# Kernel optimization log

Hardware: AMD Instinct MI355X
Metric: run time of the kernel (lower is better)

## Reference

```python
import jax, jax.numpy as jnp
import numpy as np

N = 100000       # num_nodes
E = 800000       # num edges (avg degree 8)
EMB = 64         # emb_dim
HID = 256        # hidden_dim


def setup_inputs() -> dict:
    key = jax.random.key(0)
    k1, k2, k3, k4, k5, k6, k7 = jax.random.split(key, 7)
    def xavier(k, fan_in, fan_out):
        limit = float(np.sqrt(6.0 / (fan_in + fan_out)))
        return jax.random.uniform(k, (fan_in, fan_out), jnp.float32, -limit, limit)
    return {
        "row": jax.random.randint(k1, (E,), 0, N, dtype=jnp.int64) if jax.config.jax_enable_x64 else jax.random.randint(k1, (E,), 0, N).astype(jnp.int32),
        "col": jax.random.randint(k2, (E,), 0, N).astype(jnp.int32),
        "val": jax.random.uniform(k3, (E,), jnp.float32),
        "emb": jax.random.normal(k4, (N, EMB), jnp.float32) * 0.02,
        "W0": xavier(k5, EMB, HID),
        "W1": xavier(k6, HID, HID),
        "W2": xavier(k7, HID, HID),
    }


def reference(row, col, val, emb, W0, W1, W2):
    # SpMM: out[r] = sum_{edges e with row[e]==r} val[e] * emb[col[e]]
    msgs = val[:, None] * emb[col]                      # [E, EMB] gather + scale
    x = jax.ops.segment_sum(msgs, row, num_segments=N)  # [N, EMB] scatter-add
    # MLP (bias-free linears; dropout=0.0 / eval mode => identity)
    x = jax.nn.relu(x @ W0)   # [N, HID]
    x = jax.nn.relu(x @ W1)   # [N, HID]
    x = x @ W2                # [N, HID]
    return x
```

## Files before the change

kernel.cpp:

```cpp
#include <hip/hip_runtime.h>
#include <hip/hip_bf16.h>

#define EMB 64
#define HID 256

typedef __attribute__((ext_vector_type(8))) short short8_t;
typedef __attribute__((ext_vector_type(4))) float f32x4;

__device__ __forceinline__ unsigned short f2bf(float f)
{
    union { float f; unsigned int u; } c; c.f = f;
    unsigned int u = c.u;
    u += 0x7fffu + ((u >> 16) & 1u);
    return (unsigned short)(u >> 16);
}
__device__ __forceinline__ float bf2f(unsigned short b)
{
    union { unsigned int u; float f; } c; c.u = ((unsigned int)b) << 16;
    return c.f;
}

__global__ __launch_bounds__(256) void prep_kernel(
    const float* __restrict__ emb, const float* __restrict__ W0,
    const float* __restrict__ W1, const float* __restrict__ W2,
    int* __restrict__ counts, unsigned short* __restrict__ embb,
    unsigned short* __restrict__ W0f, unsigned short* __restrict__ W1f,
    unsigned short* __restrict__ W2f, int M, int zb, int cb)
{
    int b = blockIdx.x;
    if (b < zb) {
        int idx = (b * 256 + threadIdx.x) * 4;
        if (idx + 3 < M) {
            int4 z; z.x = 0; z.y = 0; z.z = 0; z.w = 0;
            *(int4*)&counts[idx] = z;
        } else {
            for (int i = idx; i < M; ++i) counts[i] = 0;
        }
        return;
    }
    b -= zb;
    if (b < cb) {
        int idx = (b * 256 + threadIdx.x) * 4;
        if (idx + 3 < M * EMB) {
            float4 v = *(const float4*)&emb[idx];
            ushort4 o;
            o.x = f2bf(v.x); o.y = f2bf(v.y); o.z = f2bf(v.z); o.w = f2bf(v.w);
            *(ushort4*)&embb[idx] = o;
        }
        return;
    }
    b -= cb;
    if (b < 8) {
        int i    = b * 256 + threadIdx.x;
        int lane = i & 63;
        int kc   = (i >> 6) & 1;
        int nt   = i >> 7;
        int lr   = lane & 15, kg = lane >> 4;
        unsigned short tmp[8];
#pragma unroll
        for (int j = 0; j < 8; ++j)
            tmp[j] = f2bf(W0[(kc * 32 + kg * 8 + j) * HID + nt * 16 + lr]);
        *(short8_t*)&W0f[(size_t)i * 8] = *(short8_t*)tmp;
        return;
    }
    b -= 8;
    if (b < 32) {
        int i    = b * 256 + threadIdx.x;
        int lane = i & 63;
        int kc   = (i >> 6) & 7;
        int nt   = i >> 9;
        int lr   = lane & 15, kg = lane >> 4;
        unsigned short tmp[8];
#pragma unroll
        for (int j = 0; j < 8; ++j)
            tmp[j] = f2bf(W1[(kc * 32 + kg * 8 + j) * HID + nt * 16 + lr]);
        *(short8_t*)&W1f[(size_t)i * 8] = *(short8_t*)tmp;
        return;
    }
    b -= 32;
    {
        int i    = b * 256 + threadIdx.x;
        int lane = i & 63;
        int kc   = (i >> 6) & 7;
        int nt   = i >> 9;
        int lr   = lane & 15, kg = lane >> 4;
        unsigned short tmp[8];
#pragma unroll
        for (int j = 0; j < 8; ++j)
            tmp[j] = f2bf(W2[(kc * 32 + kg * 8 + j) * HID + nt * 16 + lr]);
        *(short8_t*)&W2f[(size_t)i * 8] = *(short8_t*)tmp;
    }
}

__global__ __launch_bounds__(256) void hist_kernel(
    const int* __restrict__ row, int* __restrict__ counts, int E)
{
    int base = (blockIdx.x * 256 + threadIdx.x) * 4;
    if (base + 3 < E) {
        int4 r4 = *(const int4*)&row[base];
        atomicAdd(&counts[r4.x], 1);
        atomicAdd(&counts[r4.y], 1);
        atomicAdd(&counts[r4.z], 1);
        atomicAdd(&counts[r4.w], 1);
    } else {
        for (int i = base; i < E; ++i) atomicAdd(&counts[row[i]], 1);
    }
}

__global__ __launch_bounds__(256) void scan_phase1(
    const int* __restrict__ counts, int* __restrict__ excl,
    int* __restrict__ blockSums, int n)
{
    __shared__ int s[256];
    int t = threadIdx.x;
    int base = blockIdx.x * 1024 + t * 4;
    int4 v = {0, 0, 0, 0};
    if (base + 3 < n) {
        v = *(const int4*)&counts[base];
    } else {
        if (base + 0 < n) v.x = counts[base + 0];
        if (base + 1 < n) v.y = counts[base + 1];
        if (base + 2 < n) v.z = counts[base + 2];
        if (base + 3 < n) v.w = counts[base + 3];
    }
    int tsum = v.x + v.y + v.z + v.w;
    s[t] = tsum;
    __syncthreads();
#pragma unroll
    for (int off = 1; off < 256; off <<= 1) {
        int val = (t >= off) ? s[t - off] : 0;
        __syncthreads();
        s[t] += val;
        __syncthreads();
    }
    if (t == 255) blockSums[blockIdx.x] = s[255];
    int e0 = s[t] - tsum;
    int e1 = e0 + v.x;
    int e2 = e1 + v.y;
    int e3 = e2 + v.z;
    if (base + 0 < n) excl[base + 0] = e0;
    if (base + 1 < n) excl[base + 1] = e1;
    if (base + 2 < n) excl[base + 2] = e2;
    if (base + 3 < n) excl[base + 3] = e3;
}

__global__ __launch_bounds__(256) void scan_phase2(int* blockSums, int nb)
{
    __shared__ int s[256];
    int t = threadIdx.x;
    int v = (t < nb) ? blockSums[t] : 0;
    s[t] = v;
    __syncthreads();
#pragma unroll
    for (int off = 1; off < 256; off <<= 1) {
        int val = (t >= off) ? s[t - off] : 0;
        __syncthreads();
        s[t] += val;
        __syncthreads();
    }
    if (t < nb) blockSums[t] = s[t] - v;
}

__global__ __launch_bounds__(256) void scan_phase3(
    int* __restrict__ offsets, const int* __restrict__ blockSums,
    int* __restrict__ cursor, int n)
{
    int i = blockIdx.x * 256 + threadIdx.x;
    if (i >= n) return;
    int o = offsets[i] + blockSums[i >> 10];
    offsets[i] = o;
    cursor[i]  = o;
}

__global__ __launch_bounds__(256) void scatter_kernel(
    const int* __restrict__ row, const int* __restrict__ col,
    const float* __restrict__ val, int* __restrict__ cursor,
    uint2* __restrict__ edata, int E)
{
    int e = blockIdx.x * 256 + threadIdx.x;
    if (e >= E) return;
    int r = row[e];
    int pos = atomicAdd(&cursor[r], 1);
    uint2 d;
    d.x = (unsigned)col[e];
    d.y = __float_as_uint(val[e]);
    edata[pos] = d;
}

__global__ __launch_bounds__(256) void pull_kernel(
    const int* __restrict__ offsets, const int* __restrict__ counts,
    const uint2* __restrict__ edata, const unsigned short* __restrict__ embb,
    unsigned short* __restrict__ xb, int Nn)
{
    int r    = blockIdx.x * 4 + (threadIdx.x >> 6);
    int lane = threadIdx.x & 63;
    if (r >= Nn) return;
    int beg = offsets[r];
    int cnt = counts[r];
    float acc = 0.f;
    for (int i = 0; i < cnt; i += 8) {
        uint2 ed[8];
#pragma unroll
        for (int j = 0; j < 8; ++j) {
            int idx = i + j;
            idx = (idx < cnt) ? idx : (cnt - 1);
            ed[j] = edata[beg + idx];
        }
        float g[8];
#pragma unroll
        for (int j = 0; j < 8; ++j)
            g[j] = bf2f(embb[(size_t)ed[j].x * EMB + lane]);
#pragma unroll
        for (int j = 0; j < 8; ++j) {
            float v = (i + j < cnt) ? __uint_as_float(ed[j].y) : 0.f;
            acc += v * g[j];
        }
    }
    xb[(size_t)r * EMB + lane] = f2bf(acc);
}

__global__ __launch_bounds__(256) void mlp_fused(
    const unsigned short* __restrict__ xb,
    const unsigned short* __restrict__ W0f,
    const unsigned short* __restrict__ W1f,
    const unsigned short* __restrict__ W2f,
    float* __restrict__ out, int M)
{
    __shared__ unsigned short H[64 * 256];

    const int t    = threadIdx.x;
    const int lane = t & 63;
    const int w    = t >> 6;
    const int lr   = lane & 15;
    const int kg   = lane >> 4;
    const int row0 = blockIdx.x * 64;
    char* Hb = (char*)H;

#define HOFF(row, bytecol) ((((row) * 512) + (bytecol)) ^ (((row) & 7) << 4))

    short8_t ax[2][4];
#pragma unroll
    for (int kc = 0; kc < 2; ++kc)
#pragma unroll
        for (int m = 0; m < 4; ++m) {
            int gr = row0 + m * 16 + lr;
            ax[kc][m] = *(const short8_t*)(xb + (size_t)(gr < M ? gr : 0) * EMB
                                           + kc * 32 + kg * 8);
        }
    f32x4 acc[4][4] = {};
#pragma unroll
    for (int kc = 0; kc < 2; ++kc) {
        short8_t b[4];
#pragma unroll
        for (int n = 0; n < 4; ++n)
            b[n] = *(const short8_t*)&W0f[(size_t)(((w * 4 + n) * 2 + kc) * 64 + lane) * 8];
#pragma unroll
        for (int m = 0; m < 4; ++m)
#pragma unroll
            for (int n = 0; n < 4; ++n)
                acc[m][n] = __builtin_amdgcn_mfma_f32_16x16x32_bf16(
                    ax[kc][m], b[n], acc[m][n], 0, 0, 0);
    }
#pragma unroll
    for (int m = 0; m < 4; ++m)
#pragma unroll
        for (int r = 0; r < 4; ++r)
#pragma unroll
            for (int n = 0; n < 4; ++n)
                *(unsigned short*)(Hb + HOFF(m * 16 + kg * 4 + r,
                                             (w * 64 + n * 16 + lr) * 2)) =
                    f2bf(fmaxf(acc[m][n][r], 0.f));
    __syncthreads();

    f32x4 acc2[4][4] = {};
#pragma unroll
    for (int kc = 0; kc < 8; ++kc) {
        short8_t a[4], b[4];
#pragma unroll
        for (int n = 0; n < 4; ++n)
            b[n] = *(const short8_t*)&W1f[(size_t)(((w * 4 + n) * 8 + kc) * 64 + lane) * 8];
#pragma unroll
        for (int m = 0; m < 4; ++m)
            a[m] = *(const short8_t*)(Hb + HOFF(m * 16 + lr, kc * 64 + kg * 16));
#pragma unroll
        for (int m = 0; m < 4; ++m)
#pragma unroll
            for (int n = 0; n < 4; ++n)
                acc2[m][n] = __builtin_amdgcn_mfma_f32_16x16x32_bf16(
                    a[m], b[n], acc2[m][n], 0, 0, 0);
    }
    __syncthreads();
#pragma unroll
    for (int m = 0; m < 4; ++m)
#pragma unroll
        for (int r = 0; r < 4; ++r)
#pragma unroll
            for (int n = 0; n < 4; ++n)
                *(unsigned short*)(Hb + HOFF(m * 16 + kg * 4 + r,
                                             (w * 64 + n * 16 + lr) * 2)) =
                    f2bf(fmaxf(acc2[m][n][r], 0.f));
    __syncthreads();

    f32x4 acc3[4][4] = {};
#pragma unroll
    for (int kc = 0; kc < 8; ++kc) {
        short8_t a[4], b[4];
#pragma unroll
        for (int n = 0; n < 4; ++n)
            b[n] = *(const short8_t*)&W2f[(size_t)(((w * 4 + n) * 8 + kc) * 64 + lane) * 8];
#pragma unroll
        for (int m = 0; m < 4; ++m)
            a[m] = *(const short8_t*)(Hb + HOFF(m * 16 + lr, kc * 64 + kg * 16));
#pragma unroll
        for (int m = 0; m < 4; ++m)
#pragma unroll
            for (int n = 0; n < 4; ++n)
                acc3[m][n] = __builtin_amdgcn_mfma_f32_16x16x32_bf16(
                    a[m], b[n], acc3[m][n], 0, 0, 0);
    }
#pragma unroll
    for (int m = 0; m < 4; ++m)
#pragma unroll
        for (int r = 0; r < 4; ++r) {
            int gr = row0 + m * 16 + kg * 4 + r;
            if (gr < M)
#pragma unroll
                for (int n = 0; n < 4; ++n)
                    out[(size_t)gr * HID + w * 64 + n * 16 + lr] = acc3[m][n][r];
        }
#undef HOFF
}

__global__ __launch_bounds__(256) void spmm_kernel(
    const int* __restrict__ row, const int* __restrict__ col,
    const float* __restrict__ val, const float* __restrict__ emb,
    float* __restrict__ x, int E)
{
    int gid  = blockIdx.x * blockDim.x + threadIdx.x;
    int e    = gid >> 6;
    int lane = gid & 63;
    if (e >= E) return;
    unsafeAtomicAdd(&x[(size_t)row[e] * EMB + lane],
                    val[e] * emb[(size_t)col[e] * EMB + lane]);
}

template<int K, bool RELU>
__global__ __launch_bounds__(256) void gemm_f32(
    const float* A, const float* __restrict__ B, float* C, int M)
{
    __shared__ float As[64][17];
    __shared__ float Bs[16][256];

    const int t    = threadIdx.x;
    const int tn   = t & 15;
    const int row0 = blockIdx.x * 64;
    const int sk = t & 15;
    const int sm = (t >> 4) * 4;

    float acc[4][16];
#pragma unroll
    for (int i = 0; i < 4; ++i)
#pragma unroll
        for (int j = 0; j < 16; ++j) acc[i][j] = 0.f;

    const int mB = ((t & 63) >> 4) * 4;
    const int wq = t >> 6;
    const int myM = (wq * 16) + mB;

    for (int k0 = 0; k0 < K; k0 += 16) {
        __syncthreads();
#pragma unroll
        for (int i = 0; i < 4; ++i) {
            int m  = sm + i;
            int gr = row0 + m;
            As[m][sk] = (gr < M) ? A[(size_t)gr * K + k0 + sk] : 0.f;
        }
#pragma unroll
        for (int r = 0; r < 16; ++r)
            Bs[r][t] = B[(size_t)(k0 + r) * 256 + t];
        __syncthreads();

#pragma unroll
        for (int kk = 0; kk < 16; ++kk) {
            float a0 = As[myM + 0][kk];
            float a1 = As[myM + 1][kk];
            float a2 = As[myM + 2][kk];
            float a3 = As[myM + 3][kk];
            float4 b[4];
#pragma unroll
            for (int j = 0; j < 4; ++j)
                b[j] = *(const float4*)&Bs[kk][tn * 4 + j * 64];
#pragma unroll
            for (int j = 0; j < 4; ++j) {
                acc[0][j*4+0] += a0 * b[j].x;  acc[0][j*4+1] += a0 * b[j].y;
                acc[0][j*4+2] += a0 * b[j].z;  acc[0][j*4+3] += a0 * b[j].w;
                acc[1][j*4+0] += a1 * b[j].x;  acc[1][j*4+1] += a1 * b[j].y;
                acc[1][j*4+2] += a1 * b[j].z;  acc[1][j*4+3] += a1 * b[j].w;
                acc[2][j*4+0] += a2 * b[j].x;  acc[2][j*4+1] += a2 * b[j].y;
                acc[2][j*4+2] += a2 * b[j].z;  acc[2][j*4+3] += a2 * b[j].w;
                acc[3][j*4+0] += a3 * b[j].x;  acc[3][j*4+1] += a3 * b[j].y;
                acc[3][j*4+2] += a3 * b[j].z;  acc[3][j*4+3] += a3 * b[j].w;
            }
        }
    }

#pragma unroll
    for (int i = 0; i < 4; ++i) {
        int gr = row0 + myM + i;
        if (gr < M) {
#pragma unroll
            for (int j = 0; j < 4; ++j) {
                float4 o;
                o.x = acc[i][j*4+0]; o.y = acc[i][j*4+1];
                o.z = acc[i][j*4+2]; o.w = acc[i][j*4+3];
                if (RELU) {
                    o.x = fmaxf(o.x, 0.f); o.y = fmaxf(o.y, 0.f);
                    o.z = fmaxf(o.z, 0.f); o.w = fmaxf(o.w, 0.f);
                }
                *(float4*)&C[(size_t)gr * 256 + tn * 4 + j * 64] = o;
            }
        }
    }
}

extern "C" void kernel_launch(void* const* d_in, const int* in_sizes, int n_in,
                              void* d_out, int out_size, void* d_ws, size_t ws_size,
                              hipStream_t stream)
{
    const int*   row = (const int*)d_in[0];
    const int*   col = (const int*)d_in[1];
    const float* val = (const float*)d_in[2];
    const float* emb = (const float*)d_in[3];
    const float* W0  = (const float*)d_in[4];
    const float* W1  = (const float*)d_in[5];
    const float* W2  = (const float*)d_in[6];
    float* out = (float*)d_out;

    const int E = in_sizes[0];
    const int M = in_sizes[3] / EMB;

    char* ws = (char*)d_ws;

    size_t off = 0;
    auto alloc = [&](size_t bytes) { size_t o = off; off = (off + bytes + 255) & ~(size_t)255; return o; };
    const size_t off_counts = alloc((size_t)M * 4);
    const size_t off_offs   = alloc((size_t)M * 4);
    const size_t off_cursor = alloc((size_t)M * 4);
    const size_t off_bsums  = alloc(1024);
    const size_t off_edata  = alloc((size_t)E * 8);
    const size_t off_embb   = alloc((size_t)M * EMB * 2);
    const size_t off_xb     = alloc((size_t)M * EMB * 2);
    const size_t off_w0     = alloc((size_t)EMB * HID * 2);
    const size_t off_w1     = alloc((size_t)HID * HID * 2);
    const size_t off_w2     = alloc((size_t)HID * HID * 2);
    const size_t need       = off;

    int gblocks = (M + 63) / 64;

    if (ws_size >= need) {
        int*   counts = (int*)(ws + off_counts);
        int*   offs   = (int*)(ws + off_offs);
        int*   cursor = (int*)(ws + off_cursor);
        int*   bsums  = (int*)(ws + off_bsums);
        uint2* edata  = (uint2*)(ws + off_edata);
        unsigned short* embb = (unsigned short*)(ws + off_embb);
        unsigned short* xb  = (unsigned short*)(ws + off_xb);
        unsigned short* W0f = (unsigned short*)(ws + off_w0);
        unsigned short* W1f = (unsigned short*)(ws + off_w1);
        unsigned short* W2f = (unsigned short*)(ws + off_w2);

        int zb = (M / 4 + 255) / 256;
        int cb = ((M * EMB) / 4 + 255) / 256;
        int prep_blocks = zb + cb + 8 + 32 + 32;
        prep_kernel<<<prep_blocks, 256, 0, stream>>>(
            emb, W0, W1, W2, counts, embb, W0f, W1f, W2f, M, zb, cb);

        hist_kernel<<<(E / 4 + 255) / 256, 256, 0, stream>>>(row, counts, E);
        int nb = (M + 1023) / 1024;
        scan_phase1<<<nb, 256, 0, stream>>>(counts, offs, bsums, M);
        scan_phase2<<<1, 256, 0, stream>>>(bsums, nb);
        scan_phase3<<<(M + 255) / 256, 256, 0, stream>>>(offs, bsums, cursor, M);
        scatter_kernel<<<(E + 255) / 256, 256, 0, stream>>>(row, col, val, cursor, edata, E);

        pull_kernel<<<(M + 3) / 4, 256, 0, stream>>>(offs, counts, edata, embb, xb, M);

        mlp_fused<<<gblocks, 256, 0, stream>>>(xb, W0f, W1f, W2f, out, M);
    } else {
        float* x = (float*)ws;
        (void)hipMemsetAsync(x, 0, (size_t)M * EMB * sizeof(float), stream);
        spmm_kernel<<<(E + 3) / 4, 256, 0, stream>>>(row, col, val, emb, x, E);
        gemm_f32<EMB, true ><<<gblocks, 256, 0, stream>>>(x,   W0, out, M);
        gemm_f32<HID, true ><<<gblocks, 256, 0, stream>>>(out, W1, out, M);
        gemm_f32<HID, false><<<gblocks, 256, 0, stream>>>(out, W2, out, M);
    }
}
```

Measured before the change: 201.0 us.

## Grid-stride pull kernel, halve MLP row tile, stage output through LDS

The pull kernel becomes a grid-stride loop where each wave handles about 8 rows and prefetches the next row's offset and count. The fused MLP now works on 32-row tiles instead of 64, which halves LDS and register use per block and doubles the block count. The final fp32 output is staged through shared memory so each lane writes 16-byte vectors instead of scattered 4-byte stores. Costs are an extra barrier and LDS round trip in the epilogue, and weight fragments are reloaded across twice as many blocks.

```diff
diff --git a/kernel.cpp b/kernel.cpp
--- a/kernel.cpp
+++ b/kernel.cpp
@@ -187,36 +187,46 @@
     edata[pos] = d;
 }
 
+#define ROWS_PER_WAVE 8
 __global__ __launch_bounds__(256) void pull_kernel(
     const int* __restrict__ offsets, const int* __restrict__ counts,
     const uint2* __restrict__ edata, const unsigned short* __restrict__ embb,
     unsigned short* __restrict__ xb, int Nn)
 {
-    int r    = blockIdx.x * 4 + (threadIdx.x >> 6);
-    int lane = threadIdx.x & 63;
-    if (r >= Nn) return;
-    int beg = offsets[r];
-    int cnt = counts[r];
-    float acc = 0.f;
-    for (int i = 0; i < cnt; i += 8) {
-        uint2 ed[8];
-#pragma unroll
-        for (int j = 0; j < 8; ++j) {
-            int idx = i + j;
-            idx = (idx < cnt) ? idx : (cnt - 1);
-            ed[j] = edata[beg + idx];
-        }
-        float g[8];
-#pragma unroll
-        for (int j = 0; j < 8; ++j)
-            g[j] = bf2f(embb[(size_t)ed[j].x * EMB + lane]);
-#pragma unroll
-        for (int j = 0; j < 8; ++j) {
-            float v = (i + j < cnt) ? __uint_as_float(ed[j].y) : 0.f;
-            acc += v * g[j];
-        }
-    }
-    xb[(size_t)r * EMB + lane] = f2bf(acc);
+    const int nw   = gridDim.x * 4;
+    const int wid  = blockIdx.x * 4 + (threadIdx.x >> 6);
+    const int lane = threadIdx.x & 63;
+    if (wid >= Nn) return;
+
+    int beg = offsets[wid];
+    int cnt = counts[wid];
+    for (int r = wid; r < Nn; r += nw) {
+        int rn = r + nw;
+        int begN = 0, cntN = 0;
+        if (rn < Nn) { begN = offsets[rn]; cntN = counts[rn]; }
+
+        float acc = 0.f;
+        for (int i = 0; i < cnt; i += 8) {
+            uint2 ed[8];
+#pragma unroll
+            for (int j = 0; j < 8; ++j) {
+                int idx = i + j;
+                idx = (idx < cnt) ? idx : (cnt - 1);
+                ed[j] = edata[beg + idx];
+            }
+            float g[8];
+#pragma unroll
+            for (int j = 0; j < 8; ++j)
+                g[j] = bf2f(embb[(size_t)ed[j].x * EMB + lane]);
+#pragma unroll
+            for (int j = 0; j < 8; ++j) {
+                float v = (i + j < cnt) ? __uint_as_float(ed[j].y) : 0.f;
+                acc += v * g[j];
+            }
+        }
+        xb[(size_t)r * EMB + lane] = f2bf(acc);
+        beg = begN; cnt = cntN;
+    }
 }
 
 __global__ __launch_bounds__(256) void mlp_fused(
@@ -226,28 +236,28 @@
     const unsigned short* __restrict__ W2f,
     float* __restrict__ out, int M)
 {
-    __shared__ unsigned short H[64 * 256];
+    __shared__ unsigned short H[32 * 256];
 
     const int t    = threadIdx.x;
     const int lane = t & 63;
     const int w    = t >> 6;
     const int lr   = lane & 15;
     const int kg   = lane >> 4;
-    const int row0 = blockIdx.x * 64;
+    const int row0 = blockIdx.x * 32;
     char* Hb = (char*)H;
 
 #define HOFF(row, bytecol) ((((row) * 512) + (bytecol)) ^ (((row) & 7) << 4))
 
-    short8_t ax[2][4];
+    short8_t ax[2][2];
 #pragma unroll
     for (int kc = 0; kc < 2; ++kc)
 #pragma unroll
-        for (int m = 0; m < 4; ++m) {
+        for (int m = 0; m < 2; ++m) {
             int gr = row0 + m * 16 + lr;
             ax[kc][m] = *(const short8_t*)(xb + (size_t)(gr < M ? gr : 0) * EMB
                                            + kc * 32 + kg * 8);
         }
-    f32x4 acc[4][4] = {};
+    f32x4 acc[2][4] = {};
 #pragma unroll
     for (int kc = 0; kc < 2; ++kc) {
         short8_t b[4];
@@ -255,14 +265,14 @@
         for (int n = 0; n < 4; ++n)
             b[n] = *(const short8_t*)&W0f[(size_t)(((w * 4 + n) * 2 + kc) * 64 + lane) * 8];
 #pragma unroll
-        for (int m = 0; m < 4; ++m)
+        for (int m = 0; m < 2; ++m)
 #pragma unroll
             for (int n = 0; n < 4; ++n)
                 acc[m][n] = __builtin_amdgcn_mfma_f32_16x16x32_bf16(
                     ax[kc][m], b[n], acc[m][n], 0, 0, 0);
     }
 #pragma unroll
-    for (int m = 0; m < 4; ++m)
+    for (int m = 0; m < 2; ++m)
 #pragma unroll
         for (int r = 0; r < 4; ++r)
 #pragma unroll
@@ -272,18 +282,18 @@
                     f2bf(fmaxf(acc[m][n][r], 0.f));
     __syncthreads();
 
-    f32x4 acc2[4][4] = {};
+    f32x4 acc2[2][4] = {};
 #pragma unroll
     for (int kc = 0; kc < 8; ++kc) {
-        short8_t a[4], b[4];
+        short8_t a[2], b[4];
 #pragma unroll
         for (int n = 0; n < 4; ++n)
             b[n] = *(const short8_t*)&W1f[(size_t)(((w * 4 + n) * 8 + kc) * 64 + lane) * 8];
 #pragma unroll
-        for (int m = 0; m < 4; ++m)
+        for (int m = 0; m < 2; ++m)
             a[m] = *(const short8_t*)(Hb + HOFF(m * 16 + lr, kc * 64 + kg * 16));
 #pragma unroll
-        for (int m = 0; m < 4; ++m)
+        for (int m = 0; m < 2; ++m)
 #pragma unroll
             for (int n = 0; n < 4; ++n)
                 acc2[m][n] = __builtin_amdgcn_mfma_f32_16x16x32_bf16(
@@ -291,7 +301,7 @@
     }
     __syncthreads();
 #pragma unroll
-    for (int m = 0; m < 4; ++m)
+    for (int m = 0; m < 2; ++m)
 #pragma unroll
         for (int r = 0; r < 4; ++r)
 #pragma unroll
@@ -301,33 +311,42 @@
                     f2bf(fmaxf(acc2[m][n][r], 0.f));
     __syncthreads();
 
-    f32x4 acc3[4][4] = {};
+    f32x4 acc3[2][4] = {};
 #pragma unroll
     for (int kc = 0; kc < 8; ++kc) {
-        short8_t a[4], b[4];
+        short8_t a[2], b[4];
 #pragma unroll
         for (int n = 0; n < 4; ++n)
             b[n] = *(const short8_t*)&W2f[(size_t)(((w * 4 + n) * 8 + kc) * 64 + lane) * 8];
 #pragma unroll
-        for (int m = 0; m < 4; ++m)
+        for (int m = 0; m < 2; ++m)
             a[m] = *(const short8_t*)(Hb + HOFF(m * 16 + lr, kc * 64 + kg * 16));
 #pragma unroll
-        for (int m = 0; m < 4; ++m)
+        for (int m = 0; m < 2; ++m)
 #pragma unroll
             for (int n = 0; n < 4; ++n)
                 acc3[m][n] = __builtin_amdgcn_mfma_f32_16x16x32_bf16(
                     a[m], b[n], acc3[m][n], 0, 0, 0);
     }
-#pragma unroll
-    for (int m = 0; m < 4; ++m)
-#pragma unroll
-        for (int r = 0; r < 4; ++r) {
-            int gr = row0 + m * 16 + kg * 4 + r;
+    __syncthreads();
+
+    float* Hf = (float*)H;
+#pragma unroll
+    for (int m = 0; m < 2; ++m) {
+#pragma unroll
+        for (int n = 0; n < 4; ++n)
+#pragma unroll
+            for (int r = 0; r < 4; ++r)
+                Hf[w * 1024 + (kg * 4 + r) * 64 + n * 16 + lr] = acc3[m][n][r];
+#pragma unroll
+        for (int p = 0; p < 4; ++p) {
+            int rl = (lane >> 4) + p * 4;
+            f32x4 v = *(const f32x4*)&Hf[w * 1024 + rl * 64 + (lane & 15) * 4];
+            int gr = row0 + m * 16 + rl;
             if (gr < M)
-#pragma unroll
-                for (int n = 0; n < 4; ++n)
-                    out[(size_t)gr * HID + w * 64 + n * 16 + lr] = acc3[m][n][r];
-        }
+                *(f32x4*)&out[(size_t)gr * HID + w * 64 + (lane & 15) * 4] = v;
+        }
+    }
 #undef HOFF
 }
 
@@ -455,8 +474,6 @@
     const size_t off_w2     = alloc((size_t)HID * HID * 2);
     const size_t need       = off;
 
-    int gblocks = (M + 63) / 64;
-
     if (ws_size >= need) {
         int*   counts = (int*)(ws + off_counts);
         int*   offs   = (int*)(ws + off_offs);
@@ -482,13 +499,16 @@
         scan_phase3<<<(M + 255) / 256, 256, 0, stream>>>(offs, bsums, cursor, M);
         scatter_kernel<<<(E + 255) / 256, 256, 0, stream>>>(row, col, val, cursor, edata, E);
 
-        pull_kernel<<<(M + 3) / 4, 256, 0, stream>>>(offs, counts, edata, embb, xb, M);
-
+        int pull_blocks = (M + 4 * ROWS_PER_WAVE - 1) / (4 * ROWS_PER_WAVE);
+        pull_kernel<<<pull_blocks, 256, 0, stream>>>(offs, counts, edata, embb, xb, M);
+
+        int gblocks = (M + 31) / 32;
         mlp_fused<<<gblocks, 256, 0, stream>>>(xb, W0f, W1f, W2f, out, M);
     } else {
         float* x = (float*)ws;
         (void)hipMemsetAsync(x, 0, (size_t)M * EMB * sizeof(float), stream);
         spmm_kernel<<<(E + 3) / 4, 256, 0, stream>>>(row, col, val, emb, x, E);
+        int gblocks = (M + 63) / 64;
         gemm_f32<EMB, true ><<<gblocks, 256, 0, stream>>>(x,   W0, out, M);
         gemm_f32<HID, true ><<<gblocks, 256, 0, stream>>>(out, W1, out, M);
         gemm_f32<HID, false><<<gblocks, 256, 0, stream>>>(out, W2, out, M);
```

New measurement: 195.9 us. 1.03x faster.
